# Kernel tuning notes

Measured on AMD Instinct MI355X. Metric: run time of the kernel, lower is better.

The kernel has to match this reference:

```python
import jax, jax.numpy as jnp
import numpy as np

C = 512
H_HEADS = 8
CTX_D = 768
GEO_D = 512
FFN_D = 4 * C
EPS = 1e-5


def _layernorm(x, g, b):
    mu = jnp.mean(x, axis=-1, keepdims=True)
    var = jnp.mean((x - mu) ** 2, axis=-1, keepdims=True)
    return (x - mu) * jax.lax.rsqrt(var + EPS) * g + b


def _cross_attn(x, ctx, Wq, Wk, Wv, Wo, bo, h):
    # x: (B, N, C), ctx: (B, S, Dctx)
    b, n, _ = x.shape
    s = ctx.shape[1]
    inner = Wq.shape[1]
    d = inner // h
    q = (x @ Wq).reshape(b, n, h, d)
    k = (ctx @ Wk).reshape(b, s, h, d)
    v = (ctx @ Wv).reshape(b, s, h, d)
    sim = jnp.einsum('bihd,bjhd->bhij', q, k) * (d ** -0.5)
    attn = jax.nn.softmax(sim, axis=-1)
    out = jnp.einsum('bhij,bjhd->bihd', attn, v).reshape(b, n, inner)
    return out @ Wo + bo


def setup_inputs() -> dict:
    key = jax.random.key(0)
    ks = jax.random.split(key, 24)
    std = lambda fan_in: 1.0 / np.sqrt(fan_in)
    inp = {
        'x': jax.random.normal(ks[0], (4, C, 64, 64), jnp.float32),
        'context': jax.random.normal(ks[1], (4, 77, CTX_D), jnp.float32),
        'geometry_tokens': jax.random.normal(ks[2], (4, 256, GEO_D), jnp.float32),
        # layernorm params (norm1..norm4)
        'g1': jnp.ones((C,)), 'b1': jnp.zeros((C,)),
        'g2': jnp.ones((C,)), 'b2': jnp.zeros((C,)),
        'g3': jnp.ones((C,)), 'b3': jnp.zeros((C,)),
        'g4': jnp.ones((C,)), 'b4': jnp.zeros((C,)),
        # cross-attention (context) weights
        'cWq': jax.random.normal(ks[3], (C, C)) * std(C),
        'cWk': jax.random.normal(ks[4], (CTX_D, C)) * std(CTX_D),
        'cWv': jax.random.normal(ks[5], (CTX_D, C)) * std(CTX_D),
        'cWo': jax.random.normal(ks[6], (C, C)) * std(C),
        'cbo': jnp.zeros((C,)),
        # geometry-attention weights
        'gWq': jax.random.normal(ks[7], (C, C)) * std(C),
        'gWk': jax.random.normal(ks[8], (GEO_D, C)) * std(GEO_D),
        'gWv': jax.random.normal(ks[9], (GEO_D, C)) * std(GEO_D),
        'gWo': jax.random.normal(ks[10], (C, C)) * std(C),
        'gbo': jnp.zeros((C,)),
        # FFN weights
        'W1': jax.random.normal(ks[11], (C, FFN_D)) * std(C),
        'bf1': jnp.zeros((FFN_D,)),
        'W2': jax.random.normal(ks[12], (FFN_D, C)) * std(FFN_D),
        'bf2': jnp.zeros((C,)),
    }
    return inp


def reference(x, context, geometry_tokens,
              g1, b1, g2, b2, g3, b3, g4, b4,
              cWq, cWk, cWv, cWo, cbo,
              gWq, gWk, gWv, gWo, gbo,
              W1, bf1, W2, bf2):
    b, c, h, w = x.shape
    t = x.reshape(b, c, h * w).transpose(0, 2, 1)  # (B, N, C)
    # self_attn is called with context=None -> identity, so this is t + norm1(t)
    t = t + _layernorm(t, g1, b1)
    t = t + _cross_attn(_layernorm(t, g2, b2), context, cWq, cWk, cWv, cWo, cbo, H_HEADS)
    t = t + _cross_attn(_layernorm(t, g3, b3), geometry_tokens, gWq, gWk, gWv, gWo, gbo, H_HEADS)
    hdn = jax.nn.gelu(_layernorm(t, g4, b4) @ W1 + bf1, approximate=False)
    t = t + hdn @ W2 + bf2
    return t.transpose(0, 2, 1).reshape(b, c, h, w)
```

## Files before the change

### kernel.cpp

```cpp
#include <hip/hip_runtime.h>
#include <hip/hip_bf16.h>

using bf16 = __hip_bfloat16;
typedef __attribute__((ext_vector_type(8))) short short8;
typedef __attribute__((ext_vector_type(4))) short short4v;
typedef __attribute__((ext_vector_type(4))) float floatx4;

#define DEVFN __device__ __forceinline__

DEVFN float bf2f(bf16 v) { return __bfloat162float(v); }
DEVFN bf16 f2bf(float v) { return __float2bfloat16(v); }
DEVFN float us2f(unsigned short u) {
    union { unsigned int i; float f; } c; c.i = ((unsigned int)u) << 16; return c.f;
}
DEVFN unsigned short f2bfbits(float v) {
    union { bf16 h; unsigned short u; } c; c.h = f2bf(v); return c.u;
}
DEVFN float loadF(const void* p, size_t i, int isf) {
    return isf ? ((const float*)p)[i] : us2f(((const unsigned short*)p)[i]);
}
DEVFN void gl_lds16(const bf16* g, short* l) {
    __builtin_amdgcn_global_load_lds(
        (const __attribute__((address_space(1))) unsigned int*)g,
        (__attribute__((address_space(3))) unsigned int*)l, 16, 0, 0);
}
DEVFN float fast_gelu(float v) {
    float u = v * (0.7978845608028654f + 0.0356774081f * v * v);
    float e = __expf(2.f * u);
    float th = 1.f - 2.f / (e + 1.f);
    return 0.5f * v * (1.f + th);
}

__global__ __launch_bounds__(256) void detect_kernel(const void* x, int* flag)
{
    __shared__ int any;
    if (threadIdx.x == 0) any = 0;
    __syncthreads();
    const unsigned short* p = (const unsigned short*)x;
    int hit = 0;
    for (int i = threadIdx.x; i < 8192; i += 256) {
        if ((p[i] & 0x7F80u) == 0x7F80u) hit = 1;
    }
    if (hit) any = 1;
    __syncthreads();
    if (threadIdx.x == 0) flag[0] = any;
}

__global__ __launch_bounds__(256) void convert_kernel(
    const void* __restrict__ src, bf16* __restrict__ dst, const int* __restrict__ flag, int n)
{
    int isf = *flag;
    int i = blockIdx.x * 256 + threadIdx.x;
    if (i < n) dst[i] = f2bf(loadF(src, i, isf));
}

struct SegTab {
    const void* src[12];
    int off[12];
    int cnt[12];
};
__global__ __launch_bounds__(256) void param_convert_kernel(
    SegTab tab, bf16* __restrict__ dst, const int* __restrict__ flag)
{
    int isf = *flag;
    int s = blockIdx.x;
    const void* src = tab.src[s];
    int off = tab.off[s], cnt = tab.cnt[s];
    for (int i = threadIdx.x; i < cnt; i += 256)
        dst[off + i] = f2bf(loadF(src, i, isf));
}

__global__ __launch_bounds__(256) void ln_in_kernel(
    const void* __restrict__ x, float* __restrict__ t,
    const bf16* __restrict__ g, const bf16* __restrict__ bta,
    const int* __restrict__ flag, int NN)
{
    __shared__ float tile[16][516];
    int isf = *flag;
    int b = blockIdx.y;
    int n0 = blockIdx.x * 16;
    int tid = threadIdx.x;
    int nx = tid & 15, cy = tid >> 4;
#pragma unroll
    for (int p = 0; p < 32; p++) {
        int c = p * 16 + cy;
        tile[nx][c] = loadF(x, ((size_t)b * 512 + c) * NN + n0 + nx, isf);
    }
    __syncthreads();
    int w = tid >> 6, lane = tid & 63;
    for (int rr = 0; rr < 4; rr++) {
        int r = w * 4 + rr;
        float4 v0 = *(const float4*)&tile[r][lane * 8];
        float4 v1 = *(const float4*)&tile[r][lane * 8 + 4];
        float vals[8] = {v0.x, v0.y, v0.z, v0.w, v1.x, v1.y, v1.z, v1.w};
        float s = 0.f;
#pragma unroll
        for (int i = 0; i < 8; i++) s += vals[i];
#pragma unroll
        for (int off = 32; off; off >>= 1) s += __shfl_xor(s, off, 64);
        float mu = s * (1.f / 512.f);
        float sq = 0.f;
#pragma unroll
        for (int i = 0; i < 8; i++) { float d = vals[i] - mu; sq += d * d; }
#pragma unroll
        for (int off = 32; off; off >>= 1) sq += __shfl_xor(sq, off, 64);
        float rs = rsqrtf(sq * (1.f / 512.f) + 1e-5f);
        float out[8];
#pragma unroll
        for (int i = 0; i < 8; i++) {
            int c = lane * 8 + i;
            out[i] = vals[i] + (vals[i] - mu) * rs * bf2f(g[c]) + bf2f(bta[c]);
        }
        float* tp = t + ((size_t)b * NN + n0 + r) * 512 + lane * 8;
        *(float4*)tp = make_float4(out[0], out[1], out[2], out[3]);
        *(float4*)(tp + 4) = make_float4(out[4], out[5], out[6], out[7]);
    }
}

__global__ __launch_bounds__(256) void transpose_out_kernel(
    const float* __restrict__ t, void* __restrict__ o, const int* __restrict__ flag,
    int C, int NN)
{
    __shared__ float tile[32][33];
    int isf = *flag;
    int b = blockIdx.z;
    int n0 = blockIdx.x * 32, c0 = blockIdx.y * 32;
    int tx = threadIdx.x, ty = threadIdx.y;
#pragma unroll
    for (int i = 0; i < 4; i++)
        tile[ty + i * 8][tx] = t[((size_t)b * NN + n0 + ty + i * 8) * C + c0 + tx];
    __syncthreads();
#pragma unroll
    for (int i = 0; i < 4; i++) {
        size_t oi = ((size_t)b * C + c0 + ty + i * 8) * NN + n0 + tx;
        float val = tile[tx][ty + i * 8];
        if (isf) ((float*)o)[oi] = val;
        else ((bf16*)o)[oi] = f2bf(val);
    }
}

__global__ __launch_bounds__(256) void transpose_w_kernel(
    const void* __restrict__ Wm, bf16* __restrict__ WT, const int* __restrict__ flag,
    int K, int Nc)
{
    __shared__ float tile[32][33];
    int isf = *flag;
    int n0 = blockIdx.x * 32, k0 = blockIdx.y * 32;
    int tx = threadIdx.x, ty = threadIdx.y;
#pragma unroll
    for (int i = 0; i < 4; i++)
        tile[ty + i * 8][tx] = loadF(Wm, (size_t)(k0 + ty + i * 8) * Nc + n0 + tx, isf);
    __syncthreads();
#pragma unroll
    for (int i = 0; i < 4; i++)
        WT[(size_t)(n0 + ty + i * 8) * K + k0 + tx] = f2bf(tile[tx][ty + i * 8]);
}

__global__ __launch_bounds__(256) void ln_kernel(
    const float* __restrict__ t, const bf16* __restrict__ g, const bf16* __restrict__ bta,
    bf16* __restrict__ outp, int Mrows)
{
    int w = threadIdx.x >> 6, lane = threadIdx.x & 63;
    int row = blockIdx.x * 4 + w;
    if (row >= Mrows) return;
    const float* xr = t + (size_t)row * 512;
    float4 v0 = *(const float4*)(xr + lane * 8);
    float4 v1 = *(const float4*)(xr + lane * 8 + 4);
    float vals[8] = {v0.x, v0.y, v0.z, v0.w, v1.x, v1.y, v1.z, v1.w};
    float s = 0.f;
#pragma unroll
    for (int i = 0; i < 8; i++) s += vals[i];
#pragma unroll
    for (int off = 32; off; off >>= 1) s += __shfl_xor(s, off, 64);
    float mu = s * (1.f / 512.f);
    float sq = 0.f;
#pragma unroll
    for (int i = 0; i < 8; i++) { float d = vals[i] - mu; sq += d * d; }
#pragma unroll
    for (int off = 32; off; off >>= 1) sq += __shfl_xor(sq, off, 64);
    float rs = rsqrtf(sq * (1.f / 512.f) + 1e-5f);
#pragma unroll
    for (int i = 0; i < 8; i++) {
        int c = lane * 8 + i;
        float y = (vals[i] - mu) * rs * bf2f(g[c]) + bf2f(bta[c]);
        outp[(size_t)row * 512 + c] = f2bf(y);
    }
}

template <int MODE>
__global__ __launch_bounds__(256) void gemm64(
    const bf16* __restrict__ A, const bf16* __restrict__ WT,
    const bf16* __restrict__ bias, void* __restrict__ outp,
    int M, int K, int Nc)
{
    __shared__ short As[64 * 32];
    __shared__ short Bs[64 * 32];
    const int tid = threadIdx.x;
    const int m0 = blockIdx.y * 64;
    const int n0 = blockIdx.x * 64;
    const int w = tid >> 6;
    const int lane = tid & 63;
    const int lm = lane & 15;
    const int lq = lane >> 4;

    floatx4 acc[4];
#pragma unroll
    for (int nb = 0; nb < 4; nb++) acc[nb] = (floatx4){0.f, 0.f, 0.f, 0.f};

    const int srow = tid >> 2;
    const int scol = (tid & 3) << 3;
    const int agrow = m0 + srow;
    const bool aok = agrow < M;
    const bf16* Aptr = A + (size_t)agrow * K + scol;
    const bf16* Bptr = WT + (size_t)(n0 + srow) * K + scol;

    for (int k0 = 0; k0 < K; k0 += 32) {
        __syncthreads();
        int4 av = make_int4(0, 0, 0, 0);
        if (aok) av = *(const int4*)(Aptr + k0);
        *(int4*)(&As[srow * 32 + scol]) = av;
        *(int4*)(&Bs[srow * 32 + scol]) = *(const int4*)(Bptr + k0);
        __syncthreads();
        short8 a = *(const short8*)(&As[(w * 16 + lm) * 32 + lq * 8]);
#pragma unroll
        for (int nb = 0; nb < 4; nb++) {
            short8 b = *(const short8*)(&Bs[(nb * 16 + lm) * 32 + lq * 8]);
            acc[nb] = __builtin_amdgcn_mfma_f32_16x16x32_bf16(a, b, acc[nb], 0, 0, 0);
        }
    }

#pragma unroll
    for (int nb = 0; nb < 4; nb++) {
        int col = n0 + nb * 16 + lm;
        float bv = bias ? bf2f(bias[col]) : 0.f;
#pragma unroll
        for (int r = 0; r < 4; r++) {
            int row = m0 + w * 16 + lq * 4 + r;
            if (row < M) {
                float v = acc[nb][r] + bv;
                if (MODE == 1) v = fast_gelu(v);
                if (MODE == 2) {
                    ((float*)outp)[(size_t)row * Nc + col] += v;
                } else {
                    ((bf16*)outp)[(size_t)row * Nc + col] = f2bf(v);
                }
            }
        }
    }
}

template <int MODE, int NB>
__global__ __launch_bounds__(512, 1) void gemmP(
    const bf16* __restrict__ A, const bf16* __restrict__ WT,
    const bf16* __restrict__ bias, void* __restrict__ outp,
    int K, int Nc)
{
    constexpr int BN = NB * 64;
    constexpr int ASH = 256 * 32;
    constexpr int BSH = BN * 32;
    __shared__ short As[4 * ASH];
    __shared__ short Bs[4 * BSH];

    const int tid = threadIdx.x;
    const int gx = gridDim.x;
    int g = blockIdx.y * gx + blockIdx.x;
    const int cpx = (gx * gridDim.y) >> 3;
    g = (g & 7) * cpx + (g >> 3);
    const int m0 = (g / gx) * 256;
    const int n0 = (g % gx) * BN;

    const int w = tid >> 6, lane = tid & 63;
    const int lm = lane & 15, lq = lane >> 4;
    const int wm = w >> 2, wn = w & 3;

    floatx4 acc[NB][8];
#pragma unroll
    for (int cb = 0; cb < NB; cb++)
#pragma unroll
        for (int rb = 0; rb < 8; rb++) acc[cb][rb] = (floatx4){0.f, 0.f, 0.f, 0.f};

    const int lr = lane >> 2;
    const int jg8 = (((lane & 3) ^ ((lr >> 1) & 3)) << 3);
    const bf16* gA0 = A + (size_t)(m0 + w * 16 + lr) * K + jg8;
    const bf16* gA1 = gA0 + (size_t)128 * K;
    const bf16* gB0 = WT + (size_t)(n0 + w * 16 + lr) * K + jg8;
    const bf16* gB1 = gB0 + (size_t)128 * K;

    auto STAGE = [&](int d, int koff) {
        short* la = As + d * ASH + (w * 16) * 32;
        short* lb = Bs + d * BSH + (w * 16) * 32;
        gl_lds16(gA0 + koff, la);
        gl_lds16(gA1 + koff, la + 128 * 32);
        gl_lds16(gB0 + koff, lb);
        if constexpr (NB == 4) gl_lds16(gB1 + koff, lb + 128 * 32);
    };

    const int nt = K >> 5;
    STAGE(0, 0); STAGE(1, 32); STAGE(2, 64); STAGE(3, 96);
    if constexpr (NB == 4) asm volatile("s_waitcnt vmcnt(12)\n\ts_barrier" ::: "memory");
    else                   asm volatile("s_waitcnt vmcnt(9)\n\ts_barrier" ::: "memory");

    const int fsw = ((lq ^ ((lm >> 1) & 3)) * 8);
    for (int t = 0; t < nt; ++t) {
        const short* cA = As + (t & 3) * ASH;
        const short* cB = Bs + (t & 3) * BSH;
        short8 wf[NB], xf[8];
#pragma unroll
        for (int cb = 0; cb < NB; cb++)
            wf[cb] = *(const short8*)(&cB[(wn * (NB * 16) + cb * 16 + lm) * 32 + fsw]);
#pragma unroll
        for (int rb = 0; rb < 4; rb++)
            xf[rb] = *(const short8*)(&cA[(wm * 128 + rb * 16 + lm) * 32 + fsw]);
        __builtin_amdgcn_s_setprio(1);
#pragma unroll
        for (int cb = 0; cb < NB; cb++)
#pragma unroll
            for (int rb = 0; rb < 4; rb++)
                acc[cb][rb] = __builtin_amdgcn_mfma_f32_16x16x32_bf16(wf[cb], xf[rb], acc[cb][rb], 0, 0, 0);
        __builtin_amdgcn_s_setprio(0);
#pragma unroll
        for (int rb = 4; rb < 8; rb++)
            xf[rb] = *(const short8*)(&cA[(wm * 128 + rb * 16 + lm) * 32 + fsw]);
        __builtin_amdgcn_s_setprio(1);
#pragma unroll
        for (int cb = 0; cb < NB; cb++)
#pragma unroll
            for (int rb = 4; rb < 8; rb++)
                acc[cb][rb] = __builtin_amdgcn_mfma_f32_16x16x32_bf16(wf[cb], xf[rb], acc[cb][rb], 0, 0, 0);
        __builtin_amdgcn_s_setprio(0);
        asm volatile("s_waitcnt lgkmcnt(0)\n\ts_barrier" ::: "memory");
        if (t + 4 < nt) {
            STAGE(t & 3, (t + 4) << 5);
            if constexpr (NB == 4) asm volatile("s_waitcnt vmcnt(12)\n\ts_barrier" ::: "memory");
            else                   asm volatile("s_waitcnt vmcnt(9)\n\ts_barrier" ::: "memory");
        } else if (t + 3 < nt) {
            if constexpr (NB == 4) asm volatile("s_waitcnt vmcnt(8)\n\ts_barrier" ::: "memory");
            else                   asm volatile("s_waitcnt vmcnt(6)\n\ts_barrier" ::: "memory");
        } else if (t + 2 < nt) {
            if constexpr (NB == 4) asm volatile("s_waitcnt vmcnt(4)\n\ts_barrier" ::: "memory");
            else                   asm volatile("s_waitcnt vmcnt(3)\n\ts_barrier" ::: "memory");
        } else if (t + 1 < nt) {
            asm volatile("s_waitcnt vmcnt(0)\n\ts_barrier" ::: "memory");
        }
    }

    float4 bias4[NB];
#pragma unroll
    for (int cb = 0; cb < NB; cb++) {
        if (bias) {
            const bf16* bp = bias + n0 + wn * (NB * 16) + cb * 16 + lq * 4;
            bias4[cb] = make_float4(bf2f(bp[0]), bf2f(bp[1]), bf2f(bp[2]), bf2f(bp[3]));
        } else {
            bias4[cb] = make_float4(0.f, 0.f, 0.f, 0.f);
        }
    }

    if constexpr (MODE == 2) {
        float* po = (float*)outp;
#pragma unroll
        for (int rb = 0; rb < 8; rb++) {
            size_t m = m0 + wm * 128 + rb * 16 + lm;
#pragma unroll
            for (int cb = 0; cb < NB; cb++) {
                float* p = po + m * Nc + n0 + wn * (NB * 16) + cb * 16 + lq * 4;
                float4 f = *(float4*)p;
                f.x += acc[cb][rb][0] + bias4[cb].x;
                f.y += acc[cb][rb][1] + bias4[cb].y;
                f.z += acc[cb][rb][2] + bias4[cb].z;
                f.w += acc[cb][rb][3] + bias4[cb].w;
                *(float4*)p = f;
            }
        }
    } else if constexpr (NB == 2) {
        unsigned short* op = (unsigned short*)outp;
#pragma unroll
        for (int rb = 0; rb < 8; rb++) {
            size_t m = m0 + wm * 128 + rb * 16 + lm;
#pragma unroll
            for (int cb = 0; cb < 2; cb++) {
                short4v pk;
#pragma unroll
                for (int r = 0; r < 4; r++) {
                    float vv = acc[cb][rb][r] + ((const float*)&bias4[cb])[r];
                    if (MODE == 1) vv = fast_gelu(vv);
                    pk[r] = (short)f2bfbits(vv);
                }
                *(short4v*)(op + m * Nc + n0 + wn * 32 + cb * 16 + lq * 4) = pk;
            }
        }
    } else {
        unsigned short* stgb = (unsigned short*)&As[w * 1024];
        unsigned short* op = (unsigned short*)outp;
#pragma unroll
        for (int rb = 0; rb < 8; rb++) {
#pragma unroll
            for (int cb = 0; cb < 4; cb++) {
                short4v pk;
#pragma unroll
                for (int r = 0; r < 4; r++) {
                    float vv = acc[cb][rb][r] + ((const float*)&bias4[cb])[r];
                    if (MODE == 1) vv = fast_gelu(vv);
                    pk[r] = (short)f2bfbits(vv);
                }
                int chunk = (cb * 2 + (lq >> 1)) ^ (lm & 7);
                *(short4v*)(&stgb[lm * 64 + chunk * 8 + (lq & 1) * 4]) = pk;
            }
#pragma unroll
            for (int p = 0; p < 2; p++) {
                int row = p * 8 + (lane >> 3);
                int chunk = lane & 7;
                short8 ov = *(const short8*)(&stgb[row * 64 + ((chunk ^ (row & 7)) * 8)]);
                size_t m = m0 + wm * 128 + rb * 16 + row;
                *(short8*)(op + m * Nc + n0 + wn * 64 + chunk * 8) = ov;
            }
        }
    }
}

template <int SPAD, int SVALID>
__global__ __launch_bounds__(256) void attn_mfma_kernel(
    const bf16* __restrict__ q, const bf16* __restrict__ k, const bf16* __restrict__ v,
    bf16* __restrict__ o, int N)
{
    constexpr int MB = SPAD / 16;
    constexpr int KS = SPAD / 32;
    __shared__ unsigned short lds[SPAD * 64 + 64 * SPAD];
    unsigned short* Ks = lds;
    unsigned short* Vt = lds + SPAD * 64;
    unsigned short* Pw = lds;

    const int tid = threadIdx.x;
    const int b = blockIdx.x >> 3;
    const int h = blockIdx.x & 7;
    const int n0 = blockIdx.y * 64;
    const int w = tid >> 6, lane = tid & 63;
    const int lm = lane & 15, lq = lane >> 4;

    const unsigned short* kp = (const unsigned short*)k;
    const unsigned short* vp = (const unsigned short*)v;
    for (int idx = tid * 8; idx < SPAD * 64; idx += 2048) {
        int s = idx >> 6, d0 = idx & 63;
        short8 kv = {0, 0, 0, 0, 0, 0, 0, 0};
        short8 vv = {0, 0, 0, 0, 0, 0, 0, 0};
        if (s < SVALID) {
            size_t gb = ((size_t)(b * SVALID + s)) * 512 + h * 64 + d0;
            kv = *(const short8*)(kp + gb);
            vv = *(const short8*)(vp + gb);
        }
        int kc = (d0 >> 3) ^ (s & 7);
        *(short8*)(&Ks[s * 64 + kc * 8]) = kv;
        const unsigned short* vvp = (const unsigned short*)&vv;
#pragma unroll
        for (int i = 0; i < 8; i++) {
            int d = d0 + i;
            int sc = (s >> 3) ^ (d & 7);
            Vt[d * SPAD + sc * 8 + (s & 7)] = vvp[i];
        }
    }

    const int q0 = n0 + w * 16;
    const unsigned short* qp = (const unsigned short*)q;
    size_t qbase = ((size_t)(b * N + q0 + lm)) * 512 + h * 64 + lq * 8;
    short8 qf0 = *(const short8*)(qp + qbase);
    short8 qf1 = *(const short8*)(qp + qbase + 32);
    __syncthreads();

    floatx4 sacc[MB];
#pragma unroll
    for (int mb = 0; mb < MB; mb++) sacc[mb] = (floatx4){0.f, 0.f, 0.f, 0.f};
#pragma unroll
    for (int mb = 0; mb < MB; mb++) {
        int srow = mb * 16 + lm;
        short8 a0 = *(const short8*)(&Ks[srow * 64 + ((lq ^ (lm & 7)) * 8)]);
        short8 a1 = *(const short8*)(&Ks[srow * 64 + (((4 + lq) ^ (lm & 7)) * 8)]);
        sacc[mb] = __builtin_amdgcn_mfma_f32_16x16x32_bf16(a0, qf0, sacc[mb], 0, 0, 0);
        sacc[mb] = __builtin_amdgcn_mfma_f32_16x16x32_bf16(a1, qf1, sacc[mb], 0, 0, 0);
    }

    float mx = -1e30f;
#pragma unroll
    for (int mb = 0; mb < MB; mb++)
#pragma unroll
        for (int r = 0; r < 4; r++) {
            int s = mb * 16 + lq * 4 + r;
            if (s < SVALID) mx = fmaxf(mx, sacc[mb][r]);
        }
    mx = fmaxf(mx, __shfl_xor(mx, 16, 64));
    mx = fmaxf(mx, __shfl_xor(mx, 32, 64));
    mx *= 0.125f;
    float sum = 0.f;
#pragma unroll
    for (int mb = 0; mb < MB; mb++)
#pragma unroll
        for (int r = 0; r < 4; r++) {
            int s = mb * 16 + lq * 4 + r;
            float e = (s < SVALID) ? __expf(sacc[mb][r] * 0.125f - mx) : 0.f;
            sacc[mb][r] = e;
            sum += e;
        }
    sum += __shfl_xor(sum, 16, 64);
    sum += __shfl_xor(sum, 32, 64);
    float inv = 1.f / sum;

    __syncthreads();

    unsigned short* Pme = Pw + w * 16 * SPAD;
#pragma unroll
    for (int mb = 0; mb < MB; mb++) {
        short4v pk;
        pk[0] = (short)f2bfbits(sacc[mb][0] * inv);
        pk[1] = (short)f2bfbits(sacc[mb][1] * inv);
        pk[2] = (short)f2bfbits(sacc[mb][2] * inv);
        pk[3] = (short)f2bfbits(sacc[mb][3] * inv);
        int chunk = (mb * 2 + (lq >> 1)) ^ (lm & 7);
        *(short4v*)(&Pme[lm * SPAD + chunk * 8 + (lq & 1) * 4]) = pk;
    }

    floatx4 oacc[4];
#pragma unroll
    for (int mb2 = 0; mb2 < 4; mb2++) oacc[mb2] = (floatx4){0.f, 0.f, 0.f, 0.f};
    for (int ks = 0; ks < KS; ks++) {
        int sch = ((ks * 4 + lq) ^ (lm & 7)) * 8;
        short8 bfrag = *(const short8*)(&Pme[lm * SPAD + sch]);
#pragma unroll
        for (int mb2 = 0; mb2 < 4; mb2++) {
            int d = mb2 * 16 + lm;
            short8 afrag = *(const short8*)(&Vt[d * SPAD + sch]);
            oacc[mb2] = __builtin_amdgcn_mfma_f32_16x16x32_bf16(afrag, bfrag, oacc[mb2], 0, 0, 0);
        }
    }

#pragma unroll
    for (int mb2 = 0; mb2 < 4; mb2++) {
        short4v ok;
        ok[0] = (short)f2bfbits(oacc[mb2][0]);
        ok[1] = (short)f2bfbits(oacc[mb2][1]);
        ok[2] = (short)f2bfbits(oacc[mb2][2]);
        ok[3] = (short)f2bfbits(oacc[mb2][3]);
        int chunk = (mb2 * 2 + (lq >> 1)) ^ (lm & 7);
        *(short4v*)(&Pme[lm * 64 + chunk * 8 + (lq & 1) * 4]) = ok;
    }
    unsigned short* op = (unsigned short*)o;
#pragma unroll
    for (int p = 0; p < 2; p++) {
        int row = p * 8 + (lane >> 3);
        int chunk = lane & 7;
        short8 ov = *(const short8*)(&Pme[row * 64 + ((chunk ^ (row & 7)) * 8)]);
        *(short8*)(op + ((size_t)(b * N + n0 + w * 16 + row)) * 512 + h * 64 + chunk * 8) = ov;
    }
}

extern "C" void kernel_launch(void* const* d_in, const int* in_sizes, int n_in,
                              void* d_out, int out_size, void* d_ws, size_t ws_size,
                              hipStream_t stream)
{
    const void* x   = d_in[0];
    const void* ctx = d_in[1];
    const void* geo = d_in[2];
    const void* g1 = d_in[3];  const void* b1 = d_in[4];
    const void* g2 = d_in[5];  const void* b2 = d_in[6];
    const void* g3 = d_in[7];  const void* b3 = d_in[8];
    const void* g4 = d_in[9];  const void* b4 = d_in[10];
    const void* cWq = d_in[11]; const void* cWk = d_in[12];
    const void* cWv = d_in[13]; const void* cWo = d_in[14];
    const void* cbo = d_in[15];
    const void* gWq = d_in[16]; const void* gWk = d_in[17];
    const void* gWv = d_in[18]; const void* gWo = d_in[19];
    const void* gbo = d_in[20];
    const void* W1 = d_in[21];  const void* bf1 = d_in[22];
    const void* W2 = d_in[23];  const void* bf2 = d_in[24];

    const int B = 4, C = 512, NN = 4096;
    const int M = B * NN;

    char* ws = (char*)d_ws;
    size_t off = 0;
    auto alloc = [&](size_t bytes) -> void* {
        void* p = ws + off; off += (bytes + 255) & ~(size_t)255; return p;
    };
    int*   flag = (int*)alloc(256);
    float* t  = (float*)alloc((size_t)M * C * 4);
    bf16* u   = (bf16*)alloc((size_t)M * C * 2);
    bf16* qb  = (bf16*)alloc((size_t)M * C * 2);
    bf16* kb  = (bf16*)alloc((size_t)B * 256 * C * 2);
    bf16* vb  = (bf16*)alloc((size_t)B * 256 * C * 2);
    bf16* ctxb = (bf16*)alloc((size_t)B * 77 * 768 * 2);
    bf16* geob = (bf16*)alloc((size_t)B * 256 * 512 * 2);
    bf16* cWqT = (bf16*)alloc((size_t)512 * 512 * 2);
    bf16* cWkT = (bf16*)alloc((size_t)512 * 768 * 2);
    bf16* cWvT = (bf16*)alloc((size_t)512 * 768 * 2);
    bf16* cWoT = (bf16*)alloc((size_t)512 * 512 * 2);
    bf16* gWqT = (bf16*)alloc((size_t)512 * 512 * 2);
    bf16* gWkT = (bf16*)alloc((size_t)512 * 512 * 2);
    bf16* gWvT = (bf16*)alloc((size_t)512 * 512 * 2);
    bf16* gWoT = (bf16*)alloc((size_t)512 * 512 * 2);
    bf16* W1T  = (bf16*)alloc((size_t)2048 * 512 * 2);
    bf16* W2T  = (bf16*)alloc((size_t)512 * 2048 * 2);
    bf16* prm  = (bf16*)alloc((size_t)7680 * 2);
    bf16* ob = u;

    int chunk;
    bf16* hb;
    size_t rem = (ws_size > off) ? (ws_size - off) : 0;
    if (rem >= (size_t)16384 * 2048 * 2) { chunk = 16384; hb = (bf16*)alloc((size_t)16384 * 2048 * 2); }
    else if (rem >= (size_t)8192 * 2048 * 2) { chunk = 8192; hb = (bf16*)alloc((size_t)8192 * 2048 * 2); }
    else { chunk = 4096; hb = qb; }
    (void)in_sizes; (void)n_in; (void)out_size;

    bf16 *pg1 = prm, *pb1 = prm + 512, *pg2 = prm + 1024, *pb2 = prm + 1536;
    bf16 *pg3 = prm + 2048, *pb3 = prm + 2560, *pg4 = prm + 3072, *pb4 = prm + 3584;
    bf16 *pcbo = prm + 4096, *pgbo = prm + 4608, *pbf1 = prm + 5120, *pbf2 = prm + 7168;

    dim3 tb(32, 8);

    detect_kernel<<<1, 256, 0, stream>>>(x, flag);
    SegTab tab;
    const void* srcs[12] = {g1, b1, g2, b2, g3, b3, g4, b4, cbo, gbo, bf1, bf2};
    int offs[12] = {0, 512, 1024, 1536, 2048, 2560, 3072, 3584, 4096, 4608, 5120, 7168};
    int cnts[12] = {512, 512, 512, 512, 512, 512, 512, 512, 512, 512, 2048, 512};
    for (int i = 0; i < 12; i++) { tab.src[i] = srcs[i]; tab.off[i] = offs[i]; tab.cnt[i] = cnts[i]; }
    param_convert_kernel<<<12, 256, 0, stream>>>(tab, prm, flag);
    convert_kernel<<<(B * 77 * 768 + 255) / 256, 256, 0, stream>>>(ctx, ctxb, flag, B * 77 * 768);
    convert_kernel<<<(B * 256 * 512 + 255) / 256, 256, 0, stream>>>(geo, geob, flag, B * 256 * 512);

    ln_in_kernel<<<dim3(NN / 16, B), 256, 0, stream>>>(x, t, pg1, pb1, flag, NN);

    transpose_w_kernel<<<dim3(512 / 32, 512 / 32), tb, 0, stream>>>(cWq, cWqT, flag, 512, 512);
    transpose_w_kernel<<<dim3(512 / 32, 768 / 32), tb, 0, stream>>>(cWk, cWkT, flag, 768, 512);
    transpose_w_kernel<<<dim3(512 / 32, 768 / 32), tb, 0, stream>>>(cWv, cWvT, flag, 768, 512);
    transpose_w_kernel<<<dim3(512 / 32, 512 / 32), tb, 0, stream>>>(cWo, cWoT, flag, 512, 512);
    transpose_w_kernel<<<dim3(512 / 32, 512 / 32), tb, 0, stream>>>(gWq, gWqT, flag, 512, 512);
    transpose_w_kernel<<<dim3(512 / 32, 512 / 32), tb, 0, stream>>>(gWk, gWkT, flag, 512, 512);
    transpose_w_kernel<<<dim3(512 / 32, 512 / 32), tb, 0, stream>>>(gWv, gWvT, flag, 512, 512);
    transpose_w_kernel<<<dim3(512 / 32, 512 / 32), tb, 0, stream>>>(gWo, gWoT, flag, 512, 512);
    transpose_w_kernel<<<dim3(2048 / 32, 512 / 32), tb, 0, stream>>>(W1, W1T, flag, 512, 2048);
    transpose_w_kernel<<<dim3(512 / 32, 2048 / 32), tb, 0, stream>>>(W2, W2T, flag, 2048, 512);

    ln_kernel<<<M / 4, 256, 0, stream>>>(t, pg2, pb2, u, M);
    gemmP<0, 2><<<dim3(4, M / 256), 512, 0, stream>>>(u, cWqT, nullptr, qb, 512, 512);
    gemm64<0><<<dim3(8, (308 + 63) / 64), 256, 0, stream>>>(ctxb, cWkT, nullptr, kb, 308, 768, 512);
    gemm64<0><<<dim3(8, (308 + 63) / 64), 256, 0, stream>>>(ctxb, cWvT, nullptr, vb, 308, 768, 512);
    attn_mfma_kernel<128, 77><<<dim3(B * 8, NN / 64), 256, 0, stream>>>(qb, kb, vb, ob, NN);
    gemmP<2, 2><<<dim3(4, M / 256), 512, 0, stream>>>(ob, cWoT, pcbo, t, 512, 512);

    ln_kernel<<<M / 4, 256, 0, stream>>>(t, pg3, pb3, u, M);
    gemmP<0, 2><<<dim3(4, M / 256), 512, 0, stream>>>(u, gWqT, nullptr, qb, 512, 512);
    gemm64<0><<<dim3(8, 1024 / 64), 256, 0, stream>>>(geob, gWkT, nullptr, kb, 1024, 512, 512);
    gemm64<0><<<dim3(8, 1024 / 64), 256, 0, stream>>>(geob, gWvT, nullptr, vb, 1024, 512, 512);
    attn_mfma_kernel<256, 256><<<dim3(B * 8, NN / 64), 256, 0, stream>>>(qb, kb, vb, ob, NN);
    gemmP<2, 2><<<dim3(4, M / 256), 512, 0, stream>>>(ob, gWoT, pgbo, t, 512, 512);

    ln_kernel<<<M / 4, 256, 0, stream>>>(t, pg4, pb4, u, M);
    for (int mc = 0; mc < M / chunk; mc++) {
        bf16* uc = u + (size_t)mc * chunk * 512;
        float* tc = t + (size_t)mc * chunk * 512;
        gemmP<1, 4><<<dim3(2048 / 256, chunk / 256), 512, 0, stream>>>(uc, W1T, pbf1, hb, 512, 2048);
        gemmP<2, 2><<<dim3(512 / 128, chunk / 256), 512, 0, stream>>>(hb, W2T, pbf2, tc, 2048, 512);
    }

    transpose_out_kernel<<<dim3(NN / 32, C / 32, B), tb, 0, stream>>>(t, d_out, flag, C, NN);
}
```

Baseline: 544.7 us.

## Replace GEMM main loop with double-buffered 64-wide K tiles and interleaved staging

Rewrites the big-tile GEMM kernel so each pipeline step covers 64 K-elements, using two LDS buffers instead of four 32-wide stages. Global-to-LDS loads for upcoming tiles are spread across four MFMA phases within each step. Launch bounds now request two blocks per CU. The goal is fewer barriers per unit of K and better overlap of memory traffic with MFMA work, at the cost of more complex wait-count bookkeeping and register pressure under the tighter occupancy bound.

```diff
diff --git a/kernel.cpp b/kernel.cpp
--- a/kernel.cpp
+++ b/kernel.cpp
@@ -249,17 +249,26 @@
     }
 }
 
-template <int MODE, int NB>
-__global__ __launch_bounds__(512, 1) void gemmP(
+#define MFMA_PAIR(RB, A00, A01, A10, A11)                                              \
+    _Pragma("unroll")                                                                   \
+    for (int cb = 0; cb < CB; cb++) {                                                   \
+        acc[cb][RB]     = __builtin_amdgcn_mfma_f32_16x16x32_bf16(bf0[cb], A00, acc[cb][RB], 0, 0, 0);     \
+        acc[cb][RB]     = __builtin_amdgcn_mfma_f32_16x16x32_bf16(bf1[cb], A01, acc[cb][RB], 0, 0, 0);     \
+        acc[cb][RB + 1] = __builtin_amdgcn_mfma_f32_16x16x32_bf16(bf0[cb], A10, acc[cb][RB + 1], 0, 0, 0); \
+        acc[cb][RB + 1] = __builtin_amdgcn_mfma_f32_16x16x32_bf16(bf1[cb], A11, acc[cb][RB + 1], 0, 0, 0); \
+    }
+
+template <int MODE, int CB>
+__global__ __launch_bounds__(512, 2) void gemm8p(
     const bf16* __restrict__ A, const bf16* __restrict__ WT,
     const bf16* __restrict__ bias, void* __restrict__ outp,
     int K, int Nc)
 {
-    constexpr int BN = NB * 64;
-    constexpr int ASH = 256 * 32;
-    constexpr int BSH = BN * 32;
-    __shared__ short As[4 * ASH];
-    __shared__ short Bs[4 * BSH];
+    constexpr int BN = CB * 64;
+    constexpr int ABUF = 256 * 64;
+    constexpr int BBUF = BN * 64;
+    __shared__ short As[2 * ABUF];
+    __shared__ short Bs[2 * BBUF];
 
     const int tid = threadIdx.x;
     const int gx = gridDim.x;
@@ -273,82 +282,164 @@
     const int lm = lane & 15, lq = lane >> 4;
     const int wm = w >> 2, wn = w & 3;
 
-    floatx4 acc[NB][8];
-#pragma unroll
-    for (int cb = 0; cb < NB; cb++)
+    floatx4 acc[CB][8];
+#pragma unroll
+    for (int cb = 0; cb < CB; cb++)
 #pragma unroll
         for (int rb = 0; rb < 8; rb++) acc[cb][rb] = (floatx4){0.f, 0.f, 0.f, 0.f};
 
-    const int lr = lane >> 2;
-    const int jg8 = (((lane & 3) ^ ((lr >> 1) & 3)) << 3);
-    const bf16* gA0 = A + (size_t)(m0 + w * 16 + lr) * K + jg8;
-    const bf16* gA1 = gA0 + (size_t)128 * K;
-    const bf16* gB0 = WT + (size_t)(n0 + w * 16 + lr) * K + jg8;
-    const bf16* gB1 = gB0 + (size_t)128 * K;
-
-    auto STAGE = [&](int d, int koff) {
-        short* la = As + d * ASH + (w * 16) * 32;
-        short* lb = Bs + d * BSH + (w * 16) * 32;
-        gl_lds16(gA0 + koff, la);
-        gl_lds16(gA1 + koff, la + 128 * 32);
-        gl_lds16(gB0 + koff, lb);
-        if constexpr (NB == 4) gl_lds16(gB1 + koff, lb + 128 * 32);
-    };
-
-    const int nt = K >> 5;
-    STAGE(0, 0); STAGE(1, 32); STAGE(2, 64); STAGE(3, 96);
-    if constexpr (NB == 4) asm volatile("s_waitcnt vmcnt(12)\n\ts_barrier" ::: "memory");
-    else                   asm volatile("s_waitcnt vmcnt(9)\n\ts_barrier" ::: "memory");
-
-    const int fsw = ((lq ^ ((lm >> 1) & 3)) * 8);
-    for (int t = 0; t < nt; ++t) {
-        const short* cA = As + (t & 3) * ASH;
-        const short* cB = Bs + (t & 3) * BSH;
-        short8 wf[NB], xf[8];
-#pragma unroll
-        for (int cb = 0; cb < NB; cb++)
-            wf[cb] = *(const short8*)(&cB[(wn * (NB * 16) + cb * 16 + lm) * 32 + fsw]);
-#pragma unroll
-        for (int rb = 0; rb < 4; rb++)
-            xf[rb] = *(const short8*)(&cA[(wm * 128 + rb * 16 + lm) * 32 + fsw]);
+    const int rbaseA = (tid >> 3) + ((tid >= 256) ? 96 : 0);
+    const int chk = (((tid & 7) ^ ((tid >> 3) & 7)) << 3);
+    const bf16* pA = A + (size_t)(m0 + rbaseA) * K + chk;
+    const int rbaseB = ((tid >> 7) << (CB == 4 ? 6 : 5)) + ((tid >> 3) & 15);
+    const bf16* pB = WT + (size_t)(n0 + rbaseB) * K + chk;
+    const int wbA = w * 512 + ((w >= 4) ? 6144 : 0);
+    const int wbB = (CB == 4) ? ((w >> 1) * 4096 + (w & 1) * 512)
+                              : ((w >> 1) * 2048 + (w & 1) * 512);
+    const size_t K32 = (size_t)K * 32;
+    const size_t K16 = (size_t)K * 16;
+
+    const int arow = (wm * 128 + lm) * 64;
+    const int brow = (wn * CB * 16 + lm) * 64;
+    const int sl0 = ((lq ^ (lm & 7)) << 3);
+    const int sl1 = (((4 + lq) ^ (lm & 7)) << 3);
+
+    const int nt = K >> 6;
+
+#pragma unroll
+    for (int q = 0; q < 4; q++) gl_lds16(pA + (size_t)q * K32, As + q * 2048 + wbA);
+    if constexpr (CB == 4) {
+        gl_lds16(pB,           Bs + wbB);
+        gl_lds16(pB + K16,     Bs + 1024 + wbB);
+        gl_lds16(pB + 2 * K16, Bs + 2048 + wbB);
+        gl_lds16(pB + 3 * K16, Bs + 3072 + wbB);
+    } else {
+        gl_lds16(pB,       Bs + wbB);
+        gl_lds16(pB + K16, Bs + 1024 + wbB);
+    }
+    {
+        const bf16* qA = pA + 64;
+        const bf16* qB = pB + 64;
+        if constexpr (CB == 4) {
+            gl_lds16(qB,           Bs + BBUF + wbB);
+            gl_lds16(qB + K16,     Bs + BBUF + 1024 + wbB);
+            gl_lds16(qB + 2 * K16, Bs + BBUF + 2048 + wbB);
+            gl_lds16(qB + 3 * K16, Bs + BBUF + 3072 + wbB);
+            gl_lds16(qA,           As + ABUF + wbA);
+            gl_lds16(qA + K32,     As + ABUF + 2048 + wbA);
+            asm volatile("s_waitcnt vmcnt(6)\n\ts_barrier" ::: "memory");
+        } else {
+            gl_lds16(qB,           Bs + BBUF + wbB);
+            gl_lds16(qB + K16, Bs + BBUF + 1024 + wbB);
+            gl_lds16(qA,           As + ABUF + wbA);
+            gl_lds16(qA + K32,     As + ABUF + 2048 + wbA);
+            gl_lds16(qA + 2 * K32, As + ABUF + 4096 + wbA);
+            asm volatile("s_waitcnt vmcnt(5)\n\ts_barrier" ::: "memory");
+        }
+    }
+
+    for (int s = 0; s < nt; ++s) {
+        const int cu = s & 1;
+        const short* cA = As + cu * ABUF;
+        const short* cB = Bs + cu * BBUF;
+        short* oA = As + (cu ^ 1) * ABUF;
+        short* sA = As + cu * ABUF;
+        short* sB = Bs + cu * BBUF;
+        const bf16* pA1 = pA + (s + 1) * 64;
+        const bf16* pA2 = pA + (s + 2) * 64;
+        const bf16* pB2 = pB + (s + 2) * 64;
+        short8 bf0[CB], bf1[CB], x0, x1, y0, y1;
+
+#pragma unroll
+        for (int cb = 0; cb < CB; cb++) {
+            bf0[cb] = *(const short8*)&cB[brow + cb * 1024 + sl0];
+            bf1[cb] = *(const short8*)&cB[brow + cb * 1024 + sl1];
+        }
+        x0 = *(const short8*)&cA[arow + sl0];
+        x1 = *(const short8*)&cA[arow + sl1];
+        y0 = *(const short8*)&cA[arow + 1024 + sl0];
+        y1 = *(const short8*)&cA[arow + 1024 + sl1];
+        if (s + 1 < nt) {
+            if constexpr (CB == 4) {
+                gl_lds16(pA1 + 2 * K32, oA + 2 * 2048 + wbA);
+                gl_lds16(pA1 + 3 * K32, oA + 3 * 2048 + wbA);
+            } else {
+                gl_lds16(pA1 + 3 * K32, oA + 3 * 2048 + wbA);
+            }
+        }
+        asm volatile("s_barrier" ::: "memory");
         __builtin_amdgcn_s_setprio(1);
-#pragma unroll
-        for (int cb = 0; cb < NB; cb++)
-#pragma unroll
-            for (int rb = 0; rb < 4; rb++)
-                acc[cb][rb] = __builtin_amdgcn_mfma_f32_16x16x32_bf16(wf[cb], xf[rb], acc[cb][rb], 0, 0, 0);
-        __builtin_amdgcn_s_setprio(0);
-#pragma unroll
-        for (int rb = 4; rb < 8; rb++)
-            xf[rb] = *(const short8*)(&cA[(wm * 128 + rb * 16 + lm) * 32 + fsw]);
-        __builtin_amdgcn_s_setprio(1);
-#pragma unroll
-        for (int cb = 0; cb < NB; cb++)
-#pragma unroll
-            for (int rb = 4; rb < 8; rb++)
-                acc[cb][rb] = __builtin_amdgcn_mfma_f32_16x16x32_bf16(wf[cb], xf[rb], acc[cb][rb], 0, 0, 0);
+        MFMA_PAIR(0, x0, x1, y0, y1)
         __builtin_amdgcn_s_setprio(0);
         asm volatile("s_waitcnt lgkmcnt(0)\n\ts_barrier" ::: "memory");
-        if (t + 4 < nt) {
-            STAGE(t & 3, (t + 4) << 5);
-            if constexpr (NB == 4) asm volatile("s_waitcnt vmcnt(12)\n\ts_barrier" ::: "memory");
-            else                   asm volatile("s_waitcnt vmcnt(9)\n\ts_barrier" ::: "memory");
-        } else if (t + 3 < nt) {
-            if constexpr (NB == 4) asm volatile("s_waitcnt vmcnt(8)\n\ts_barrier" ::: "memory");
-            else                   asm volatile("s_waitcnt vmcnt(6)\n\ts_barrier" ::: "memory");
-        } else if (t + 2 < nt) {
-            if constexpr (NB == 4) asm volatile("s_waitcnt vmcnt(4)\n\ts_barrier" ::: "memory");
-            else                   asm volatile("s_waitcnt vmcnt(3)\n\ts_barrier" ::: "memory");
-        } else if (t + 1 < nt) {
-            asm volatile("s_waitcnt vmcnt(0)\n\ts_barrier" ::: "memory");
-        }
-    }
-
-    float4 bias4[NB];
-#pragma unroll
-    for (int cb = 0; cb < NB; cb++) {
+
+        x0 = *(const short8*)&cA[arow + 2 * 1024 + sl0];
+        x1 = *(const short8*)&cA[arow + 2 * 1024 + sl1];
+        y0 = *(const short8*)&cA[arow + 3 * 1024 + sl0];
+        y1 = *(const short8*)&cA[arow + 3 * 1024 + sl1];
+        if (s + 2 < nt) {
+            gl_lds16(pB2,       sB + wbB);
+            gl_lds16(pB2 + K16, sB + 1024 + wbB);
+        }
+        asm volatile("s_barrier" ::: "memory");
+        __builtin_amdgcn_s_setprio(1);
+        MFMA_PAIR(2, x0, x1, y0, y1)
+        __builtin_amdgcn_s_setprio(0);
+        asm volatile("s_waitcnt lgkmcnt(0)\n\ts_barrier" ::: "memory");
+
+        x0 = *(const short8*)&cA[arow + 4 * 1024 + sl0];
+        x1 = *(const short8*)&cA[arow + 4 * 1024 + sl1];
+        y0 = *(const short8*)&cA[arow + 5 * 1024 + sl0];
+        y1 = *(const short8*)&cA[arow + 5 * 1024 + sl1];
+        if (s + 2 < nt) {
+            if constexpr (CB == 4) {
+                gl_lds16(pB2 + 2 * K16, sB + 2048 + wbB);
+                gl_lds16(pB2 + 3 * K16, sB + 3072 + wbB);
+            } else {
+                gl_lds16(pA2, sA + wbA);
+            }
+        }
+        asm volatile("s_barrier" ::: "memory");
+        __builtin_amdgcn_s_setprio(1);
+        MFMA_PAIR(4, x0, x1, y0, y1)
+        __builtin_amdgcn_s_setprio(0);
+        asm volatile("s_waitcnt lgkmcnt(0)\n\ts_barrier" ::: "memory");
+
+        x0 = *(const short8*)&cA[arow + 6 * 1024 + sl0];
+        x1 = *(const short8*)&cA[arow + 6 * 1024 + sl1];
+        y0 = *(const short8*)&cA[arow + 7 * 1024 + sl0];
+        y1 = *(const short8*)&cA[arow + 7 * 1024 + sl1];
+        if (s + 2 < nt) {
+            if constexpr (CB == 4) {
+                gl_lds16(pA2,       sA + wbA);
+                gl_lds16(pA2 + K32, sA + 2048 + wbA);
+            } else {
+                gl_lds16(pA2 + K32,     sA + 2048 + wbA);
+                gl_lds16(pA2 + 2 * K32, sA + 4096 + wbA);
+            }
+        }
+        asm volatile("s_barrier" ::: "memory");
+        __builtin_amdgcn_s_setprio(1);
+        MFMA_PAIR(6, x0, x1, y0, y1)
+        __builtin_amdgcn_s_setprio(0);
+        if (s <= nt - 3) {
+            if constexpr (CB == 4)
+                asm volatile("s_waitcnt vmcnt(6) lgkmcnt(0)\n\ts_barrier" ::: "memory");
+            else
+                asm volatile("s_waitcnt vmcnt(5) lgkmcnt(0)\n\ts_barrier" ::: "memory");
+        } else if (s == nt - 2) {
+            asm volatile("s_waitcnt vmcnt(0) lgkmcnt(0)\n\ts_barrier" ::: "memory");
+        } else {
+            asm volatile("s_waitcnt lgkmcnt(0)\n\ts_barrier" ::: "memory");
+        }
+    }
+    __syncthreads();
+
+    float4 bias4[CB];
+#pragma unroll
+    for (int cb = 0; cb < CB; cb++) {
         if (bias) {
-            const bf16* bp = bias + n0 + wn * (NB * 16) + cb * 16 + lq * 4;
+            const bf16* bp = bias + n0 + wn * (CB * 16) + cb * 16 + lq * 4;
             bias4[cb] = make_float4(bf2f(bp[0]), bf2f(bp[1]), bf2f(bp[2]), bf2f(bp[3]));
         } else {
             bias4[cb] = make_float4(0.f, 0.f, 0.f, 0.f);
@@ -361,8 +452,8 @@
         for (int rb = 0; rb < 8; rb++) {
             size_t m = m0 + wm * 128 + rb * 16 + lm;
 #pragma unroll
-            for (int cb = 0; cb < NB; cb++) {
-                float* p = po + m * Nc + n0 + wn * (NB * 16) + cb * 16 + lq * 4;
+            for (int cb = 0; cb < CB; cb++) {
+                float* p = po + m * Nc + n0 + wn * (CB * 16) + cb * 16 + lq * 4;
                 float4 f = *(float4*)p;
                 f.x += acc[cb][rb][0] + bias4[cb].x;
                 f.y += acc[cb][rb][1] + bias4[cb].y;
@@ -371,7 +462,7 @@
                 *(float4*)p = f;
             }
         }
-    } else if constexpr (NB == 2) {
+    } else if constexpr (CB == 2) {
         unsigned short* op = (unsigned short*)outp;
 #pragma unroll
         for (int rb = 0; rb < 8; rb++) {
@@ -637,25 +728,25 @@
     transpose_w_kernel<<<dim3(512 / 32, 2048 / 32), tb, 0, stream>>>(W2, W2T, flag, 2048, 512);
 
     ln_kernel<<<M / 4, 256, 0, stream>>>(t, pg2, pb2, u, M);
-    gemmP<0, 2><<<dim3(4, M / 256), 512, 0, stream>>>(u, cWqT, nullptr, qb, 512, 512);
+    gemm8p<0, 2><<<dim3(4, M / 256), 512, 0, stream>>>(u, cWqT, nullptr, qb, 512, 512);
     gemm64<0><<<dim3(8, (308 + 63) / 64), 256, 0, stream>>>(ctxb, cWkT, nullptr, kb, 308, 768, 512);
     gemm64<0><<<dim3(8, (308 + 63) / 64), 256, 0, stream>>>(ctxb, cWvT, nullptr, vb, 308, 768, 512);
     attn_mfma_kernel<128, 77><<<dim3(B * 8, NN / 64), 256, 0, stream>>>(qb, kb, vb, ob, NN);
-    gemmP<2, 2><<<dim3(4, M / 256), 512, 0, stream>>>(ob, cWoT, pcbo, t, 512, 512);
+    gemm8p<2, 2><<<dim3(4, M / 256), 512, 0, stream>>>(ob, cWoT, pcbo, t, 512, 512);
 
     ln_kernel<<<M / 4, 256, 0, stream>>>(t, pg3, pb3, u, M);
-    gemmP<0, 2><<<dim3(4, M / 256), 512, 0, stream>>>(u, gWqT, nullptr, qb, 512, 512);
+    gemm8p<0, 2><<<dim3(4, M / 256), 512, 0, stream>>>(u, gWqT, nullptr, qb, 512, 512);
     gemm64<0><<<dim3(8, 1024 / 64), 256, 0, stream>>>(geob, gWkT, nullptr, kb, 1024, 512, 512);
     gemm64<0><<<dim3(8, 1024 / 64), 256, 0, stream>>>(geob, gWvT, nullptr, vb, 1024, 512, 512);
     attn_mfma_kernel<256, 256><<<dim3(B * 8, NN / 64), 256, 0, stream>>>(qb, kb, vb, ob, NN);
-    gemmP<2, 2><<<dim3(4, M / 256), 512, 0, stream>>>(ob, gWoT, pgbo, t, 512, 512);
+    gemm8p<2, 2><<<dim3(4, M / 256), 512, 0, stream>>>(ob, gWoT, pgbo, t, 512, 512);
 
     ln_kernel<<<M / 4, 256, 0, stream>>>(t, pg4, pb4, u, M);
     for (int mc = 0; mc < M / chunk; mc++) {
         bf16* uc = u + (size_t)mc * chunk * 512;
         float* tc = t + (size_t)mc * chunk * 512;
-        gemmP<1, 4><<<dim3(2048 / 256, chunk / 256), 512, 0, stream>>>(uc, W1T, pbf1, hb, 512, 2048);
-        gemmP<2, 2><<<dim3(512 / 128, chunk / 256), 512, 0, stream>>>(hb, W2T, pbf2, tc, 2048, 512);
+        gemm8p<1, 4><<<dim3(2048 / 256, chunk / 256), 512, 0, stream>>>(uc, W1T, pbf1, hb, 512, 2048);
+        gemm8p<2, 2><<<dim3(512 / 128, chunk / 256), 512, 0, stream>>>(hb, W2T, pbf2, tc, 2048, 512);
     }
 
     transpose_out_kernel<<<dim3(NN / 32, C / 32, B), tb, 0, stream>>>(t, d_out, flag, C, NN);
```

Measured after the change: 516.7 us. 5.1% less time.
